# Kernel optimization log

Measured on AMD Instinct MI355X. Metric: run time of the kernel, lower is better.

The kernel has to match this reference:

```python
import jax, jax.numpy as jnp
import numpy as np

N, E, D_IN, H = 100000, 1000000, 128, 64


def setup_inputs() -> dict:
    key = jax.random.key(0)
    ks = jax.random.split(key, 8)
    return {
        "x": jax.random.normal(ks[0], (N, D_IN), dtype=jnp.float32),
        "edge_index": jax.random.randint(ks[1], (2, E), 0, N, dtype=jnp.int64),
        "W1": jax.random.normal(ks[2], (H, D_IN), dtype=jnp.float32) * (1.0 / np.sqrt(D_IN)),
        "b1": jax.random.normal(ks[3], (H,), dtype=jnp.float32) * 0.05,
        "Wmu": jax.random.normal(ks[4], (H, H), dtype=jnp.float32) * (1.0 / np.sqrt(H)),
        "bmu": jax.random.normal(ks[5], (H,), dtype=jnp.float32) * 0.05,
        "Wlv": jax.random.normal(ks[6], (H, H), dtype=jnp.float32) * (1.0 / np.sqrt(H)),
        "blv": jax.random.normal(ks[7], (H,), dtype=jnp.float32) * 0.05,
    }


def reference(x, edge_index, W1, b1, Wmu, bmu, Wlv, blv):
    n = x.shape[0]
    # GCNConv (PyG defaults): add self-loops, symmetric normalization
    loop = jnp.arange(n, dtype=edge_index.dtype)
    src = jnp.concatenate([edge_index[0], loop])  # [E+N]
    dst = jnp.concatenate([edge_index[1], loop])  # [E+N]
    deg = jax.ops.segment_sum(jnp.ones(src.shape[0], dtype=x.dtype), dst, num_segments=n)
    dinv = jnp.where(deg > 0, jax.lax.rsqrt(deg), 0.0)  # deg^{-1/2}
    norm = dinv[src] * dinv[dst]  # [E+N]
    h = x @ W1.T  # [N, H] linear transform before aggregation
    msg = h[src] * norm[:, None]  # gather + scale, [E+N, H]
    agg = jax.ops.segment_sum(msg, dst, num_segments=n) + b1  # scatter-add + bias
    h = jax.nn.relu(agg)
    return (h @ Wmu.T + bmu, h @ Wlv.T + blv)
```

## Files before the change

### kernel.cpp

```cpp
#include <hip/hip_runtime.h>

#define DIN 128
#define HDIM 64
#define SLAB 32
#define OVF_CAP 65536
#define EPT 3

__device__ __forceinline__ unsigned short f2bf(float f) {
    unsigned u = __float_as_uint(f);
    unsigned r = (u + 0x7fffu + ((u >> 16) & 1u)) >> 16;
    return (unsigned short)r;
}
__device__ __forceinline__ float lo16f(unsigned v) { return __uint_as_float(v << 16); }
__device__ __forceinline__ float hi16f(unsigned v) { return __uint_as_float(v & 0xffff0000u); }

__global__ __launch_bounds__(256) void k_front(
        const int* __restrict__ src, const int* __restrict__ dst,
        int* __restrict__ cursor, int* __restrict__ slab,
        int* __restrict__ ovf, int* __restrict__ govf, int E,
        const float* __restrict__ x, const float* __restrict__ W1,
        unsigned short* __restrict__ hs_bf, int n) {
    __shared__ float4 xs[64 * 16];
    __shared__ float4 ws[64 * 16];
    int t = threadIdx.x;
    int bid = blockIdx.x;
    int ty = t >> 4, tx = t & 15;
    int nodeBase = bid * 64;

    int ebase = bid * (256 * EPT) + t;
    int d[EPT], s[EPT], p[EPT];
    bool ok[EPT];
    #pragma unroll
    for (int q = 0; q < EPT; ++q) {
        int e = ebase + q * 256;
        ok[q] = e < E;
        d[q] = ok[q] ? dst[e] : 0;
        s[q] = ok[q] ? src[e] : 0;
    }

    const float4* W14 = (const float4*)W1;
    const float4* x4 = (const float4*)(x + (size_t)nodeBase * DIN);
    int limf4 = (n - nodeBase) * (DIN / 4);
    float4 wg[2][4], xg[2][4];
    #pragma unroll
    for (int c = 0; c < 2; ++c)
        #pragma unroll
        for (int i = 0; i < 4; ++i) {
            int e = t + i * 256;
            int r = e >> 4, c4 = e & 15;
            int f4 = r * 32 + c * 16 + c4;
            wg[c][i] = W14[f4];
            xg[c][i] = (f4 < limf4) ? x4[f4] : make_float4(0.f, 0.f, 0.f, 0.f);
        }

    #pragma unroll
    for (int q = 0; q < EPT; ++q)
        if (ok[q]) p[q] = atomicAdd(&cursor[d[q]], 1);

    float acc[4][4] = {};
    #pragma unroll
    for (int c = 0; c < 2; ++c) {
        if (c) __syncthreads();
        #pragma unroll
        for (int i = 0; i < 4; ++i) {
            int e = t + i * 256;
            int r = e >> 4, c4 = e & 15;
            ws[r * 16 + (c4 ^ (r & 15))] = wg[c][i];
            xs[r * 16 + (c4 ^ (r & 15))] = xg[c][i];
        }
        __syncthreads();
        #pragma unroll 8
        for (int k4 = 0; k4 < 16; ++k4) {
            float4 xa[4], wb[4];
            #pragma unroll
            for (int i = 0; i < 4; ++i) {
                int r = ty + 16 * i;
                xa[i] = xs[r * 16 + (k4 ^ (r & 15))];
            }
            #pragma unroll
            for (int j = 0; j < 4; ++j) {
                int r = tx + 16 * j;
                wb[j] = ws[r * 16 + (k4 ^ (r & 15))];
            }
            #pragma unroll
            for (int i = 0; i < 4; ++i)
                #pragma unroll
                for (int j = 0; j < 4; ++j)
                    acc[i][j] += xa[i].x * wb[j].x + xa[i].y * wb[j].y +
                                 xa[i].z * wb[j].z + xa[i].w * wb[j].w;
        }
    }

    #pragma unroll
    for (int q = 0; q < EPT; ++q) {
        if (ok[q]) {
            if (p[q] < SLAB) {
                slab[(size_t)d[q] * SLAB + p[q]] = s[q];
            } else {
                int o = atomicAdd(govf, 1);
                if (o < OVF_CAP) { ovf[2 * o] = d[q]; ovf[2 * o + 1] = s[q]; }
            }
        }
    }

    #pragma unroll
    for (int i = 0; i < 4; ++i) {
        int node = nodeBase + ty + 16 * i;
        if (node < n) {
            #pragma unroll
            for (int j = 0; j < 4; ++j)
                hs_bf[(size_t)node * HDIM + tx + 16 * j] = f2bf(acc[i][j]);
        }
    }
}

__global__ __launch_bounds__(256) void k_scale(const int* __restrict__ cursor,
                                               unsigned short* __restrict__ hs_bf, int n) {
    int t = blockIdx.x * 256 + threadIdx.x;
    int node = t >> 3;
    if (node >= n) return;
    float dn = rsqrtf((float)cursor[node] + 1.0f);
    unsigned* p = (unsigned*)(hs_bf + ((size_t)node << 6) + 8 * (t & 7));
    uint4 v = *(uint4*)p;
    uint4 o;
    o.x = (unsigned)f2bf(lo16f(v.x) * dn) | ((unsigned)f2bf(hi16f(v.x) * dn) << 16);
    o.y = (unsigned)f2bf(lo16f(v.y) * dn) | ((unsigned)f2bf(hi16f(v.y) * dn) << 16);
    o.z = (unsigned)f2bf(lo16f(v.z) * dn) | ((unsigned)f2bf(hi16f(v.z) * dn) << 16);
    o.w = (unsigned)f2bf(lo16f(v.w) * dn) | ((unsigned)f2bf(hi16f(v.w) * dn) << 16);
    *(uint4*)p = o;
}

__global__ __launch_bounds__(256) void k_gather(const int* __restrict__ cursor,
                                                const int* __restrict__ slab,
                                                const unsigned short* __restrict__ hs_bf,
                                                float* __restrict__ h, int n) {
    int tid = threadIdx.x;
    int lane = tid & 63, wave = tid >> 6;
    int grp = lane >> 3;
    int w8 = lane & 7;
    const int NPW = 8;
    int base = blockIdx.x * (4 * NPW) + wave * NPW;
    for (int nn = 0; nn < NPW; ++nn) {
        int node = base + nn;
        if (node >= n) break;
        int c = cursor[node];
        int cs = (c < SLAB) ? c : SLAB;
        int sv = (lane < cs) ? slab[(size_t)node * SLAB + lane] : 0;
        uint4 v0 = *(const uint4*)(hs_bf + ((size_t)node << 6) + 8 * w8);
        float sw = (grp == 0) ? 1.f : 0.f;
        float a0 = sw * lo16f(v0.x), a1 = sw * hi16f(v0.x);
        float a2 = sw * lo16f(v0.y), a3 = sw * hi16f(v0.y);
        float a4 = sw * lo16f(v0.z), a5 = sw * hi16f(v0.z);
        float a6 = sw * lo16f(v0.w), a7 = sw * hi16f(v0.w);
        int nfull = cs >> 3;
        for (int q = 0; q < nfull; ++q) {
            int s = __shfl(sv, 8 * q + grp);
            uint4 v = *(const uint4*)(hs_bf + ((size_t)s << 6) + 8 * w8);
            a0 += lo16f(v.x); a1 += hi16f(v.x);
            a2 += lo16f(v.y); a3 += hi16f(v.y);
            a4 += lo16f(v.z); a5 += hi16f(v.z);
            a6 += lo16f(v.w); a7 += hi16f(v.w);
        }
        int r = cs & 7;
        if (r) {
            int e = 8 * nfull + grp;
            float wt = (grp < r) ? 1.f : 0.f;
            int s = __shfl(sv, (e < SLAB) ? e : 0);
            uint4 v = *(const uint4*)(hs_bf + ((size_t)s << 6) + 8 * w8);
            a0 += wt * lo16f(v.x); a1 += wt * hi16f(v.x);
            a2 += wt * lo16f(v.y); a3 += wt * hi16f(v.y);
            a4 += wt * lo16f(v.z); a5 += wt * hi16f(v.z);
            a6 += wt * lo16f(v.w); a7 += wt * hi16f(v.w);
        }
        #define RED(A) A += __shfl_xor(A, 8); A += __shfl_xor(A, 16); A += __shfl_xor(A, 32);
        RED(a0) RED(a1) RED(a2) RED(a3) RED(a4) RED(a5) RED(a6) RED(a7)
        #undef RED
        if (lane < 8) {
            float* hp = h + ((size_t)node << 6) + 8 * w8;
            *(float4*)hp = make_float4(a0, a1, a2, a3);
            *(float4*)(hp + 4) = make_float4(a4, a5, a6, a7);
        }
    }
}

__global__ __launch_bounds__(256) void k_overflow(const int* __restrict__ govf,
                                                  const int* __restrict__ ovf,
                                                  const unsigned short* __restrict__ hs_bf,
                                                  float* __restrict__ h) {
    int novf = govf[0];
    if (novf > OVF_CAP) novf = OVF_CAP;
    int wid = (blockIdx.x * 256 + threadIdx.x) >> 6;
    int lane = threadIdx.x & 63;
    int nw = (gridDim.x * 256) >> 6;
    for (int i = wid; i < novf; i += nw) {
        int d = ovf[2 * i], s = ovf[2 * i + 1];
        atomicAdd(&h[(size_t)d * HDIM + lane],
                  lo16f((unsigned)hs_bf[(size_t)s * HDIM + lane]));
    }
}

__global__ __launch_bounds__(256) void k_out(const float* __restrict__ h,
                                             const int* __restrict__ cursor,
                                             const float* __restrict__ b1,
                                             const float* __restrict__ Wmu,
                                             const float* __restrict__ bmu,
                                             const float* __restrict__ Wlv,
                                             const float* __restrict__ blv,
                                             float* __restrict__ out, int n) {
    __shared__ float4 xs[64 * 16];
    __shared__ uint2 wsb[128 * 16];
    int t = threadIdx.x;
    int ty = t >> 4;
    int tx = t & 15;
    int nodeBase = blockIdx.x * 64;

    #pragma unroll
    for (int i = 0; i < 8; ++i) {
        int e = t + i * 256;
        int r = e >> 4, c4 = e & 15;
        const float4* Wr = (r < 64) ? ((const float4*)Wmu + r * 16)
                                    : ((const float4*)Wlv + (r - 64) * 16);
        float4 wv = Wr[c4];
        uint2 pk;
        pk.x = (unsigned)f2bf(wv.x) | ((unsigned)f2bf(wv.y) << 16);
        pk.y = (unsigned)f2bf(wv.z) | ((unsigned)f2bf(wv.w) << 16);
        wsb[r * 16 + (c4 ^ (r & 15))] = pk;
    }
    const float4* h4 = (const float4*)(h + (size_t)nodeBase * HDIM);
    int limf4 = (n - nodeBase) * (HDIM / 4);
    #pragma unroll
    for (int i = 0; i < 4; ++i) {
        int f = t + i * 256;
        int r = f >> 4, c4 = f & 15;
        float4 v = make_float4(0.f, 0.f, 0.f, 0.f);
        if (f < limf4) {
            v = h4[f];
            float dn = rsqrtf((float)cursor[nodeBase + r] + 1.0f);
            float4 bb = ((const float4*)b1)[c4];
            v.x = fmaxf(fmaf(v.x, dn, bb.x), 0.f);
            v.y = fmaxf(fmaf(v.y, dn, bb.y), 0.f);
            v.z = fmaxf(fmaf(v.z, dn, bb.z), 0.f);
            v.w = fmaxf(fmaf(v.w, dn, bb.w), 0.f);
        }
        xs[r * 16 + (c4 ^ (r & 15))] = v;
    }
    float bias[8];
    #pragma unroll
    for (int j = 0; j < 8; ++j) {
        int o = tx + 16 * j;
        bias[j] = (o < 64) ? bmu[o] : blv[o - 64];
    }
    __syncthreads();

    float acc[4][8] = {};
    #pragma unroll 4
    for (int k4 = 0; k4 < 16; ++k4) {
        float4 xa[4];
        #pragma unroll
        for (int i = 0; i < 4; ++i) {
            int r = ty + 16 * i;
            xa[i] = xs[r * 16 + (k4 ^ (r & 15))];
        }
        #pragma unroll
        for (int j = 0; j < 8; ++j) {
            int r = tx + 16 * j;
            uint2 wv = wsb[r * 16 + (k4 ^ (r & 15))];
            float w0 = lo16f(wv.x), w1 = hi16f(wv.x);
            float w2 = lo16f(wv.y), w3 = hi16f(wv.y);
            #pragma unroll
            for (int i = 0; i < 4; ++i)
                acc[i][j] += xa[i].x * w0 + xa[i].y * w1 + xa[i].z * w2 + xa[i].w * w3;
        }
    }
    #pragma unroll
    for (int i = 0; i < 4; ++i) {
        int node = nodeBase + ty + 16 * i;
        if (node < n) {
            #pragma unroll
            for (int j = 0; j < 8; ++j) {
                int o = tx + 16 * j;
                float val = acc[i][j] + bias[j];
                if (o < 64)
                    out[(size_t)node * HDIM + o] = val;
                else
                    out[(size_t)n * HDIM + (size_t)node * HDIM + (o - 64)] = val;
            }
        }
    }
}

extern "C" void kernel_launch(void* const* d_in, const int* in_sizes, int n_in,
                              void* d_out, int out_size, void* d_ws, size_t ws_size,
                              hipStream_t stream) {
    const float* x   = (const float*)d_in[0];
    const int*   ei  = (const int*)d_in[1];
    const float* W1  = (const float*)d_in[2];
    const float* b1  = (const float*)d_in[3];
    const float* Wmu = (const float*)d_in[4];
    const float* bmu = (const float*)d_in[5];
    const float* Wlv = (const float*)d_in[6];
    const float* blv = (const float*)d_in[7];
    float* out = (float*)d_out;

    const int N = in_sizes[0] / DIN;
    const int E = in_sizes[1] / 2;
    const int* src = ei;
    const int* dst = ei + E;

    auto align256 = [](size_t b) { return (b + 255) & ~(size_t)255; };
    char* ws = (char*)d_ws;
    size_t off = 0;
    int* cursor = (int*)(ws + off); off += align256((size_t)N * 4);
    int* govf   = (int*)(ws + off); off += 256;
    int* slab   = (int*)(ws + off); off += align256((size_t)N * SLAB * 4);
    int* ovf    = (int*)(ws + off); off += align256((size_t)OVF_CAP * 2 * 4);
    unsigned short* hs_bf = (unsigned short*)(ws + off);
    off += align256((size_t)N * HDIM * 2);
    float* h = (float*)(ws + off); off += align256((size_t)N * HDIM * 4);

    hipMemsetAsync(cursor, 0, align256((size_t)N * 4) + 256, stream);

    int blocks = (N + 63) / 64;
    k_front<<<blocks, 256, 0, stream>>>(src, dst, cursor, slab, ovf, govf, E,
                                        x, W1, hs_bf, N);
    k_scale<<<(N * 8 + 255) / 256, 256, 0, stream>>>(cursor, hs_bf, N);
    k_gather<<<(N + 31) / 32, 256, 0, stream>>>(cursor, slab, hs_bf, h, N);
    k_overflow<<<8, 256, 0, stream>>>(govf, ovf, hs_bf, h);
    k_out<<<(N + 63) / 64, 256, 0, stream>>>(h, cursor, b1, Wmu, bmu, Wlv, blv, out, N);
}
```

Baseline: 161.8 us.

## Split front kernel into interleaved scatter/GEMM blocks, fold scaling into gather, store bf16 aggregate

The front kernel now interleaves dedicated edge-scatter blocks (5 per cycle) with GEMM blocks (8 per cycle) instead of having each block do both jobs. The separate degree-scaling kernel is removed: the gather looks up each neighbour's degree and applies the per-source normalisation on the fly. The aggregated hidden state is stored as bf16 rather than fp32 to halve its traffic. The overflow kernel becomes a single serial wave doing read-modify-write in bf16, which avoids atomics but is slow if there are many overflow edges and adds bf16 rounding error.

```diff
diff --git a/kernel.cpp b/kernel.cpp
--- a/kernel.cpp
+++ b/kernel.cpp
@@ -4,7 +4,6 @@
 #define HDIM 64
 #define SLAB 32
 #define OVF_CAP 65536
-#define EPT 3
 
 __device__ __forceinline__ unsigned short f2bf(float f) {
     unsigned u = __float_as_uint(f);
@@ -17,56 +16,65 @@
 __global__ __launch_bounds__(256) void k_front(
         const int* __restrict__ src, const int* __restrict__ dst,
         int* __restrict__ cursor, int* __restrict__ slab,
-        int* __restrict__ ovf, int* __restrict__ govf, int E,
+        int* __restrict__ ovf, int* __restrict__ govf, int E, int scBlocks,
         const float* __restrict__ x, const float* __restrict__ W1,
-        unsigned short* __restrict__ hs_bf, int n) {
+        unsigned short* __restrict__ hs_bf, int n, int gBlocks) {
     __shared__ float4 xs[64 * 16];
     __shared__ float4 ws[64 * 16];
     int t = threadIdx.x;
-    int bid = blockIdx.x;
+    int cyc = blockIdx.x / 13, r = blockIdx.x % 13;
+
+    if (r < 5) {
+        int sid = cyc * 5 + r;
+        if (sid >= scBlocks) return;
+        int ebase = sid * 1024 + t;
+        int d[4], s[4], p[4];
+        bool ok[4];
+        #pragma unroll
+        for (int q = 0; q < 4; ++q) {
+            int e = ebase + q * 256;
+            ok[q] = e < E;
+            d[q] = ok[q] ? dst[e] : 0;
+            s[q] = ok[q] ? src[e] : 0;
+        }
+        #pragma unroll
+        for (int q = 0; q < 4; ++q)
+            if (ok[q]) p[q] = atomicAdd(&cursor[d[q]], 1);
+        #pragma unroll
+        for (int q = 0; q < 4; ++q) {
+            if (ok[q]) {
+                if (p[q] < SLAB) {
+                    slab[(size_t)d[q] * SLAB + p[q]] = s[q];
+                } else {
+                    int o = atomicAdd(govf, 1);
+                    if (o < OVF_CAP) { ovf[2 * o] = d[q]; ovf[2 * o + 1] = s[q]; }
+                }
+            }
+        }
+        return;
+    }
+
+    int gid = cyc * 8 + (r - 5);
+    if (gid >= gBlocks) return;
     int ty = t >> 4, tx = t & 15;
-    int nodeBase = bid * 64;
-
-    int ebase = bid * (256 * EPT) + t;
-    int d[EPT], s[EPT], p[EPT];
-    bool ok[EPT];
-    #pragma unroll
-    for (int q = 0; q < EPT; ++q) {
-        int e = ebase + q * 256;
-        ok[q] = e < E;
-        d[q] = ok[q] ? dst[e] : 0;
-        s[q] = ok[q] ? src[e] : 0;
-    }
-
+    int nodeBase = gid * 64;
     const float4* W14 = (const float4*)W1;
     const float4* x4 = (const float4*)(x + (size_t)nodeBase * DIN);
     int limf4 = (n - nodeBase) * (DIN / 4);
-    float4 wg[2][4], xg[2][4];
-    #pragma unroll
-    for (int c = 0; c < 2; ++c)
+
+    float acc[4][4] = {};
+    #pragma unroll
+    for (int c = 0; c < 2; ++c) {
+        if (c) __syncthreads();
         #pragma unroll
         for (int i = 0; i < 4; ++i) {
             int e = t + i * 256;
-            int r = e >> 4, c4 = e & 15;
-            int f4 = r * 32 + c * 16 + c4;
-            wg[c][i] = W14[f4];
-            xg[c][i] = (f4 < limf4) ? x4[f4] : make_float4(0.f, 0.f, 0.f, 0.f);
-        }
-
-    #pragma unroll
-    for (int q = 0; q < EPT; ++q)
-        if (ok[q]) p[q] = atomicAdd(&cursor[d[q]], 1);
-
-    float acc[4][4] = {};
-    #pragma unroll
-    for (int c = 0; c < 2; ++c) {
-        if (c) __syncthreads();
-        #pragma unroll
-        for (int i = 0; i < 4; ++i) {
-            int e = t + i * 256;
-            int r = e >> 4, c4 = e & 15;
-            ws[r * 16 + (c4 ^ (r & 15))] = wg[c][i];
-            xs[r * 16 + (c4 ^ (r & 15))] = xg[c][i];
+            int rr = e >> 4, c4 = e & 15;
+            int f4 = rr * 32 + c * 16 + c4;
+            ws[rr * 16 + (c4 ^ (rr & 15))] = W14[f4];
+            float4 v = make_float4(0.f, 0.f, 0.f, 0.f);
+            if (f4 < limf4) v = x4[f4];
+            xs[rr * 16 + (c4 ^ (rr & 15))] = v;
         }
         __syncthreads();
         #pragma unroll 8
@@ -74,13 +82,13 @@
             float4 xa[4], wb[4];
             #pragma unroll
             for (int i = 0; i < 4; ++i) {
-                int r = ty + 16 * i;
-                xa[i] = xs[r * 16 + (k4 ^ (r & 15))];
+                int rr = ty + 16 * i;
+                xa[i] = xs[rr * 16 + (k4 ^ (rr & 15))];
             }
             #pragma unroll
             for (int j = 0; j < 4; ++j) {
-                int r = tx + 16 * j;
-                wb[j] = ws[r * 16 + (k4 ^ (r & 15))];
+                int rr = tx + 16 * j;
+                wb[j] = ws[rr * 16 + (k4 ^ (rr & 15))];
             }
             #pragma unroll
             for (int i = 0; i < 4; ++i)
@@ -90,19 +98,6 @@
                                  xa[i].z * wb[j].z + xa[i].w * wb[j].w;
         }
     }
-
-    #pragma unroll
-    for (int q = 0; q < EPT; ++q) {
-        if (ok[q]) {
-            if (p[q] < SLAB) {
-                slab[(size_t)d[q] * SLAB + p[q]] = s[q];
-            } else {
-                int o = atomicAdd(govf, 1);
-                if (o < OVF_CAP) { ovf[2 * o] = d[q]; ovf[2 * o + 1] = s[q]; }
-            }
-        }
-    }
-
     #pragma unroll
     for (int i = 0; i < 4; ++i) {
         int node = nodeBase + ty + 16 * i;
@@ -114,26 +109,10 @@
     }
 }
 
-__global__ __launch_bounds__(256) void k_scale(const int* __restrict__ cursor,
-                                               unsigned short* __restrict__ hs_bf, int n) {
-    int t = blockIdx.x * 256 + threadIdx.x;
-    int node = t >> 3;
-    if (node >= n) return;
-    float dn = rsqrtf((float)cursor[node] + 1.0f);
-    unsigned* p = (unsigned*)(hs_bf + ((size_t)node << 6) + 8 * (t & 7));
-    uint4 v = *(uint4*)p;
-    uint4 o;
-    o.x = (unsigned)f2bf(lo16f(v.x) * dn) | ((unsigned)f2bf(hi16f(v.x) * dn) << 16);
-    o.y = (unsigned)f2bf(lo16f(v.y) * dn) | ((unsigned)f2bf(hi16f(v.y) * dn) << 16);
-    o.z = (unsigned)f2bf(lo16f(v.z) * dn) | ((unsigned)f2bf(hi16f(v.z) * dn) << 16);
-    o.w = (unsigned)f2bf(lo16f(v.w) * dn) | ((unsigned)f2bf(hi16f(v.w) * dn) << 16);
-    *(uint4*)p = o;
-}
-
 __global__ __launch_bounds__(256) void k_gather(const int* __restrict__ cursor,
                                                 const int* __restrict__ slab,
                                                 const unsigned short* __restrict__ hs_bf,
-                                                float* __restrict__ h, int n) {
+                                                unsigned short* __restrict__ h_bf, int n) {
     int tid = threadIdx.x;
     int lane = tid & 63, wave = tid >> 6;
     int grp = lane >> 3;
@@ -145,9 +124,15 @@
         if (node >= n) break;
         int c = cursor[node];
         int cs = (c < SLAB) ? c : SLAB;
-        int sv = (lane < cs) ? slab[(size_t)node * SLAB + lane] : 0;
+        int sv = 0;
+        float dnv = 0.f;
+        if (lane < cs) {
+            sv = slab[(size_t)node * SLAB + lane];
+            dnv = rsqrtf((float)cursor[sv] + 1.0f);
+        }
+        float dni = rsqrtf((float)c + 1.0f);
         uint4 v0 = *(const uint4*)(hs_bf + ((size_t)node << 6) + 8 * w8);
-        float sw = (grp == 0) ? 1.f : 0.f;
+        float sw = (grp == 0) ? dni : 0.f;
         float a0 = sw * lo16f(v0.x), a1 = sw * hi16f(v0.x);
         float a2 = sw * lo16f(v0.y), a3 = sw * hi16f(v0.y);
         float a4 = sw * lo16f(v0.z), a5 = sw * hi16f(v0.z);
@@ -155,51 +140,58 @@
         int nfull = cs >> 3;
         for (int q = 0; q < nfull; ++q) {
             int s = __shfl(sv, 8 * q + grp);
+            float dn = __shfl(dnv, 8 * q + grp);
             uint4 v = *(const uint4*)(hs_bf + ((size_t)s << 6) + 8 * w8);
-            a0 += lo16f(v.x); a1 += hi16f(v.x);
-            a2 += lo16f(v.y); a3 += hi16f(v.y);
-            a4 += lo16f(v.z); a5 += hi16f(v.z);
-            a6 += lo16f(v.w); a7 += hi16f(v.w);
-        }
-        int r = cs & 7;
-        if (r) {
+            a0 = fmaf(dn, lo16f(v.x), a0); a1 = fmaf(dn, hi16f(v.x), a1);
+            a2 = fmaf(dn, lo16f(v.y), a2); a3 = fmaf(dn, hi16f(v.y), a3);
+            a4 = fmaf(dn, lo16f(v.z), a4); a5 = fmaf(dn, hi16f(v.z), a5);
+            a6 = fmaf(dn, lo16f(v.w), a6); a7 = fmaf(dn, hi16f(v.w), a7);
+        }
+        int rm = cs & 7;
+        if (rm) {
             int e = 8 * nfull + grp;
-            float wt = (grp < r) ? 1.f : 0.f;
-            int s = __shfl(sv, (e < SLAB) ? e : 0);
+            int idx = (e < SLAB) ? e : 0;
+            float wt = (grp < rm) ? 1.f : 0.f;
+            int s = __shfl(sv, idx);
+            float dn = wt * __shfl(dnv, idx);
             uint4 v = *(const uint4*)(hs_bf + ((size_t)s << 6) + 8 * w8);
-            a0 += wt * lo16f(v.x); a1 += wt * hi16f(v.x);
-            a2 += wt * lo16f(v.y); a3 += wt * hi16f(v.y);
-            a4 += wt * lo16f(v.z); a5 += wt * hi16f(v.z);
-            a6 += wt * lo16f(v.w); a7 += wt * hi16f(v.w);
+            a0 = fmaf(dn, lo16f(v.x), a0); a1 = fmaf(dn, hi16f(v.x), a1);
+            a2 = fmaf(dn, lo16f(v.y), a2); a3 = fmaf(dn, hi16f(v.y), a3);
+            a4 = fmaf(dn, lo16f(v.z), a4); a5 = fmaf(dn, hi16f(v.z), a5);
+            a6 = fmaf(dn, lo16f(v.w), a6); a7 = fmaf(dn, hi16f(v.w), a7);
         }
         #define RED(A) A += __shfl_xor(A, 8); A += __shfl_xor(A, 16); A += __shfl_xor(A, 32);
         RED(a0) RED(a1) RED(a2) RED(a3) RED(a4) RED(a5) RED(a6) RED(a7)
         #undef RED
         if (lane < 8) {
-            float* hp = h + ((size_t)node << 6) + 8 * w8;
-            *(float4*)hp = make_float4(a0, a1, a2, a3);
-            *(float4*)(hp + 4) = make_float4(a4, a5, a6, a7);
-        }
-    }
-}
-
-__global__ __launch_bounds__(256) void k_overflow(const int* __restrict__ govf,
-                                                  const int* __restrict__ ovf,
-                                                  const unsigned short* __restrict__ hs_bf,
-                                                  float* __restrict__ h) {
+            uint4 pk;
+            pk.x = (unsigned)f2bf(a0) | ((unsigned)f2bf(a1) << 16);
+            pk.y = (unsigned)f2bf(a2) | ((unsigned)f2bf(a3) << 16);
+            pk.z = (unsigned)f2bf(a4) | ((unsigned)f2bf(a5) << 16);
+            pk.w = (unsigned)f2bf(a6) | ((unsigned)f2bf(a7) << 16);
+            *(uint4*)(h_bf + ((size_t)node << 6) + 8 * w8) = pk;
+        }
+    }
+}
+
+__global__ __launch_bounds__(64) void k_overflow(const int* __restrict__ govf,
+                                                 const int* __restrict__ ovf,
+                                                 const int* __restrict__ cursor,
+                                                 const unsigned short* __restrict__ hs_bf,
+                                                 unsigned short* __restrict__ h_bf) {
     int novf = govf[0];
     if (novf > OVF_CAP) novf = OVF_CAP;
-    int wid = (blockIdx.x * 256 + threadIdx.x) >> 6;
-    int lane = threadIdx.x & 63;
-    int nw = (gridDim.x * 256) >> 6;
-    for (int i = wid; i < novf; i += nw) {
+    int lane = threadIdx.x;
+    for (int i = 0; i < novf; ++i) {
         int d = ovf[2 * i], s = ovf[2 * i + 1];
-        atomicAdd(&h[(size_t)d * HDIM + lane],
-                  lo16f((unsigned)hs_bf[(size_t)s * HDIM + lane]));
-    }
-}
-
-__global__ __launch_bounds__(256) void k_out(const float* __restrict__ h,
+        float dn = rsqrtf((float)cursor[s] + 1.0f);
+        float hv = lo16f((unsigned)h_bf[(size_t)d * HDIM + lane]);
+        float av = lo16f((unsigned)hs_bf[(size_t)s * HDIM + lane]);
+        h_bf[(size_t)d * HDIM + lane] = f2bf(fmaf(dn, av, hv));
+    }
+}
+
+__global__ __launch_bounds__(256) void k_out(const unsigned short* __restrict__ h_bf,
                                              const int* __restrict__ cursor,
                                              const float* __restrict__ b1,
                                              const float* __restrict__ Wmu,
@@ -226,7 +218,6 @@
         pk.y = (unsigned)f2bf(wv.z) | ((unsigned)f2bf(wv.w) << 16);
         wsb[r * 16 + (c4 ^ (r & 15))] = pk;
     }
-    const float4* h4 = (const float4*)(h + (size_t)nodeBase * HDIM);
     int limf4 = (n - nodeBase) * (HDIM / 4);
     #pragma unroll
     for (int i = 0; i < 4; ++i) {
@@ -234,13 +225,13 @@
         int r = f >> 4, c4 = f & 15;
         float4 v = make_float4(0.f, 0.f, 0.f, 0.f);
         if (f < limf4) {
-            v = h4[f];
+            uint2 hv = *(const uint2*)(h_bf + (size_t)nodeBase * HDIM + 4 * (size_t)f);
             float dn = rsqrtf((float)cursor[nodeBase + r] + 1.0f);
             float4 bb = ((const float4*)b1)[c4];
-            v.x = fmaxf(fmaf(v.x, dn, bb.x), 0.f);
-            v.y = fmaxf(fmaf(v.y, dn, bb.y), 0.f);
-            v.z = fmaxf(fmaf(v.z, dn, bb.z), 0.f);
-            v.w = fmaxf(fmaf(v.w, dn, bb.w), 0.f);
+            v.x = fmaxf(fmaf(lo16f(hv.x), dn, bb.x), 0.f);
+            v.y = fmaxf(fmaf(hi16f(hv.x), dn, bb.y), 0.f);
+            v.z = fmaxf(fmaf(lo16f(hv.y), dn, bb.z), 0.f);
+            v.w = fmaxf(fmaf(hi16f(hv.y), dn, bb.w), 0.f);
         }
         xs[r * 16 + (c4 ^ (r & 15))] = v;
     }
@@ -316,15 +307,18 @@
     int* ovf    = (int*)(ws + off); off += align256((size_t)OVF_CAP * 2 * 4);
     unsigned short* hs_bf = (unsigned short*)(ws + off);
     off += align256((size_t)N * HDIM * 2);
-    float* h = (float*)(ws + off); off += align256((size_t)N * HDIM * 4);
+    unsigned short* h_bf = (unsigned short*)(ws + off);
+    off += align256((size_t)N * HDIM * 2);
 
     hipMemsetAsync(cursor, 0, align256((size_t)N * 4) + 256, stream);
 
-    int blocks = (N + 63) / 64;
-    k_front<<<blocks, 256, 0, stream>>>(src, dst, cursor, slab, ovf, govf, E,
-                                        x, W1, hs_bf, N);
-    k_scale<<<(N * 8 + 255) / 256, 256, 0, stream>>>(cursor, hs_bf, N);
-    k_gather<<<(N + 31) / 32, 256, 0, stream>>>(cursor, slab, hs_bf, h, N);
-    k_overflow<<<8, 256, 0, stream>>>(govf, ovf, hs_bf, h);
-    k_out<<<(N + 63) / 64, 256, 0, stream>>>(h, cursor, b1, Wmu, bmu, Wlv, blv, out, N);
-}
+    int scBlocks = (E + 1023) / 1024;
+    int gBlocks  = (N + 63) / 64;
+    int cycles = max((scBlocks + 4) / 5, (gBlocks + 7) / 8);
+    k_front<<<cycles * 13, 256, 0, stream>>>(src, dst, cursor, slab, ovf, govf,
+                                             E, scBlocks, x, W1, hs_bf, N, gBlocks);
+    k_gather<<<(N + 31) / 32, 256, 0, stream>>>(cursor, slab, hs_bf, h_bf, N);
+    k_overflow<<<1, 64, 0, stream>>>(govf, ovf, cursor, hs_bf, h_bf);
+    k_out<<<(N + 63) / 64, 256, 0, stream>>>(h_bf, cursor, b1, Wmu, bmu, Wlv, blv,
+                                             out, N);
+}
```

After: 147.5 us. 1.1x faster.
